# Kernel optimization log

Hardware: AMD Instinct MI355X
Metric: run time of the kernel (lower is better)

Reference implementation:

```python
import jax, jax.numpy as jnp
import numpy as np

V, E, H, K, PAD = 30000, 128, 256, 32, 0
B, T = 128, 512


def _lstm_dir(x, W_ih, W_hh, b, reverse):
    # x: [B,T,E]; PyTorch LSTM gate order i,f,g,o. b = b_ih + b_hh (mathematically identical).
    Bb, Hh = x.shape[0], W_hh.shape[1]
    xg = jnp.einsum('bte,ge->btg', x, W_ih) + b          # [B,T,4H] precomputed input gates
    xg = jnp.swapaxes(xg, 0, 1)                          # [T,B,4H]

    def step(carry, xg_t):
        h, c = carry
        g = xg_t + h @ W_hh.T
        i, f, gc, o = jnp.split(g, 4, axis=-1)
        c = jax.nn.sigmoid(f) * c + jax.nn.sigmoid(i) * jnp.tanh(gc)
        h = jax.nn.sigmoid(o) * jnp.tanh(c)
        return (h, c), h

    init = (jnp.zeros((Bb, Hh), x.dtype), jnp.zeros((Bb, Hh), x.dtype))
    _, hs = jax.lax.scan(step, init, xg, reverse=reverse)
    return jnp.swapaxes(hs, 0, 1)                        # [B,T,H]


def _viterbi(em, mask, start, end, trans):
    # torchcrf-style Viterbi decode. em: [B,T,K], mask: [B,T] bool (mask[:,0] all True).
    Bb, Tt, Kk = em.shape
    score0 = start[None, :] + em[:, 0]                   # [B,K]
    em_t = jnp.swapaxes(em, 0, 1)[1:]                    # [T-1,B,K]
    m_t = jnp.swapaxes(mask, 0, 1)[1:]                   # [T-1,B]

    def step(score, inp):
        e, m = inp
        cand = score[:, :, None] + trans[None] + e[:, None, :]   # [B,K,K]
        nxt = cand.max(axis=1)
        idx = cand.argmax(axis=1).astype(jnp.int32)               # backpointers [B,K]
        score = jnp.where(m[:, None], nxt, score)
        return score, idx

    score, hist = jax.lax.scan(step, score0, (em_t, m_t))         # hist: [T-1,B,K]
    score = score + end[None, :]
    best = jnp.argmax(score, axis=1).astype(jnp.int32)            # [B] tag at seq end
    barange = jnp.arange(Bb)

    def back(b, inp):
        idx, m = inp
        nb = jnp.where(m, idx[barange, b], b)
        return nb, nb

    _, tags_prev = jax.lax.scan(back, best, (hist, m_t), reverse=True)  # [T-1,B]
    tags = jnp.concatenate([tags_prev, best[None]], axis=0)             # [T,B]
    return jnp.swapaxes(tags, 0, 1)                                     # [B,T] int32


def setup_inputs() -> dict:
    key = jax.random.key(0)
    ks = jax.random.split(key, 14)
    s = 0.1
    f32 = jnp.float32
    return {
        'input': jax.random.randint(ks[0], (B, T), 0, V),
        'mask': jnp.ones((B, T), dtype=bool),
        'target': jax.random.randint(ks[1], (B, T), 0, K),
        'embed_table': jax.random.normal(ks[2], (V, E), f32) * s,
        'W_ih_f': jax.random.normal(ks[3], (4 * H, E), f32) * s,
        'W_hh_f': jax.random.normal(ks[4], (4 * H, H), f32) * s,
        'b_f': jax.random.normal(ks[5], (4 * H,), f32) * s,
        'W_ih_b': jax.random.normal(ks[6], (4 * H, E), f32) * s,
        'W_hh_b': jax.random.normal(ks[7], (4 * H, H), f32) * s,
        'b_b': jax.random.normal(ks[8], (4 * H,), f32) * s,
        'linear_w': jax.random.normal(ks[9], (K, 2 * H), f32) * s,
        'linear_b': jax.random.normal(ks[10], (K,), f32) * s,
        'start_trans': jax.random.normal(ks[11], (K,), f32) * s,
        'end_trans': jax.random.normal(ks[12], (K,), f32) * s,
        'transitions': jax.random.normal(ks[13], (K, K), f32) * s,
    }


def reference(input, mask, target, embed_table, W_ih_f, W_hh_f, b_f,
              W_ih_b, W_hh_b, b_b, linear_w, linear_b,
              start_trans, end_trans, transitions):
    # target is only used by loss_fn; forward() is decode, so it is unused here.
    table = embed_table.at[PAD].set(0.0)                 # padding_idx row is zero
    x = table[input]                                     # [B,T,E]
    hf = _lstm_dir(x, W_ih_f, W_hh_f, b_f, reverse=False)
    hb = _lstm_dir(x, W_ih_b, W_hh_b, b_b, reverse=True)
    h = jnp.concatenate([hf, hb], axis=-1)               # [B,T,2H]
    em = jnp.einsum('bth,kh->btk', h, linear_w) + linear_b  # emissions [B,T,K]
    return _viterbi(em, mask, start_trans, end_trans, transitions)
```

## Files before the change

### kernel.cpp

```cpp
#include <hip/hip_runtime.h>
#include <stdint.h>

#define BB 128
#define TT 512
#define EE 128
#define HH 256
#define KK 32
#define ASTRD 386
#define WSTR  388
#define MAGIC 0x13572468

typedef double f64x4 __attribute__((ext_vector_type(4)));

#define OFF_CNT (512ull << 10)
#define OFF_FLG (516ull << 10)
#define OFF_EM  (2ull << 20)

__global__ __launch_bounds__(512, 1) void k_persist(
        const int* __restrict__ tok, const float* __restrict__ table,
        const float* __restrict__ Wihf, const float* __restrict__ Whhf,
        const float* __restrict__ bf,
        const float* __restrict__ Wihb, const float* __restrict__ Whhb,
        const float* __restrict__ bb,
        const float* __restrict__ lw,
        float* __restrict__ hx, int* __restrict__ cnt,
        double* __restrict__ em, int* __restrict__ flags) {
    __shared__ __align__(16) double Ah[16 * ASTRD];
    __shared__ __align__(16) float  Wl[64 * WSTR];
    __shared__ float Gl[16 * 66];
    __shared__ float Lw[2 * 256];

    const int tid  = threadIdx.x;
    const int blk  = blockIdx.x;
    const int grp  = blk & 15;
    const int dir  = grp >> 3;
    const int tile = grp & 7;
    const int hsl  = blk >> 4;
    const int b0   = tile * 16;
    const int u0   = hsl * 16;
    int* mycnt = cnt + grp * 64;

    if (blk == 0 && tid == 0) flags[8] = MAGIC;

    const float* Wih = dir ? Wihb : Wihf;
    const float* Whh = dir ? Whhb : Whhf;
    const float* bia = dir ? bb : bf;

    for (int idx = tid; idx < 64 * 384; idx += 512) {
        int c = idx / 384;
        int k = idx - c * 384;
        int grow = (c >> 4) * HH + u0 + (c & 15);
        float v = (k < EE) ? Wih[(size_t)grow * EE + k]
                           : Whh[(size_t)grow * HH + (k - EE)];
        Wl[c * WSTR + k] = v;
    }
    {
        int i = tid;
        Lw[i] = lw[(size_t)(hsl * 2 + (i >> 8)) * (2 * HH) + dir * HH + (i & 255)];
    }

    const int l = tid & 63;
    const int w = tid >> 6;

    int mode = 0;
    int rowIdx[4] = {0, 0, 0, 0}, colIdx[4] = {0, 0, 0, 0};
    int mAi = l & 15, kAi = l >> 4, nBi = l & 15, kBi = l >> 4;
    {
        f64x4 z; z[0] = 0.0; z[1] = 0.0; z[2] = 0.0; z[3] = 0.0;
        f64x4 d1 = __builtin_amdgcn_mfma_f64_16x16x4f64((double)l, 1.0, z, 0, 0, 0);
        f64x4 d2 = __builtin_amdgcn_mfma_f64_16x16x4f64(1.0, (double)l, z, 0, 0, 0);
        bool am = true, ak = true, bm = true, bk = true;
        int rm[4], rk[4], cm[4], ck[4];
#pragma unroll
        for (int r = 0; r < 4; ++r) {
            const int v1 = (int)d1[r], v2 = (int)d2[r];
            const bool e1 = ((double)v1 == d1[r]);
            const bool e2 = ((double)v2 == d2[r]);
            rm[r] = (v1 - 96) >> 2;
            am = am && e1 && (((v1 - 96) & 3) == 0) && rm[r] >= 0 && rm[r] < 16;
            rk[r] = (v1 - 6) >> 4;
            ak = ak && e1 && (((v1 - 6) & 15) == 0) && rk[r] >= 0 && rk[r] < 16;
            cm[r] = (v2 - 96) >> 2;
            bm = bm && e2 && (((v2 - 96) & 3) == 0) && cm[r] >= 0 && cm[r] < 16;
            ck[r] = (v2 - 6) >> 4;
            bk = bk && e2 && (((v2 - 6) & 15) == 0) && ck[r] >= 0 && ck[r] < 16;
        }
        const bool Am = (__ballot(am ? 1 : 0) == ~0ull);
        const bool Ak = (__ballot(ak ? 1 : 0) == ~0ull);
        const bool Bm = (__ballot(bm ? 1 : 0) == ~0ull);
        const bool Bk = (__ballot(bk ? 1 : 0) == ~0ull);
        if ((Am || Ak) && (Bm || Bk)) {
            mAi = Am ? (l & 15) : (l >> 2);
            kAi = Am ? (l >> 4) : (l & 3);
            nBi = Bm ? (l & 15) : (l >> 2);
            kBi = Bm ? (l >> 4) : (l & 3);
            f64x4 d3 = __builtin_amdgcn_mfma_f64_16x16x4f64(
                (double)kAi, (double)(1 << kBi), z, 0, 0, 0);
            const bool k34 = (d3[0] == 34.0) && (d3[1] == 34.0) &&
                             (d3[2] == 34.0) && (d3[3] == 34.0);
            if (__ballot(k34 ? 1 : 0) == ~0ull) {
                mode = 1;
#pragma unroll
                for (int r = 0; r < 4; ++r) {
                    rowIdx[r] = Am ? rm[r] : rk[r];
                    colIdx[r] = Bm ? cm[r] : ck[r];
                }
            }
        }
    }

    const int c = tid & 63;
    const float* WrowL = Wl + c * WSTR;
    const float bias_c = bia[(c >> 4) * HH + u0 + (c & 15)];

    const double* Arow = Ah + mAi * ASTRD;
    const float*  Wb   = Wl + (w * 16 + nBi) * WSTR + kBi;
    int   glIdx[4];
    float biasv[4];
#pragma unroll
    for (int r = 0; r < 4; ++r) {
        glIdx[r] = rowIdx[r] * 66 + w * 16 + colIdx[r];
        biasv[r] = bia[w * HH + u0 + colIdx[r]];
    }

    const int er = tid >> 4, eu = tid & 15;
    float c_state = 0.f;
    long guard = 0;
    float xgv[2];
    float xgm[4];

    for (int s = 0; s <= TT; ++s) {
        if (s < TT) {
            const int t = dir ? (TT - 1 - s) : s;
            const int i = tid;
            const int r = i >> 5, e4 = i & 31;
            int tk = tok[(b0 + r) * TT + t];
            float4 v = make_float4(0.f, 0.f, 0.f, 0.f);
            if (tk != 0) v = ((const float4*)(table + (size_t)tk * EE))[e4];
            double2* dst = (double2*)(Ah + r * ASTRD + e4 * 4);
            dst[0] = make_double2((double)v.x, (double)v.y);
            dst[1] = make_double2((double)v.z, (double)v.w);
        }
        __syncthreads();

        if (s < TT) {
            if (mode != 0) {
                if (w < 4) {
                    f64x4 ax0; ax0[0]=0.0; ax0[1]=0.0; ax0[2]=0.0; ax0[3]=0.0;
                    f64x4 ax1 = ax0;
#pragma unroll 8
                    for (int kb = 0; kb < 32; kb += 2) {
                        double a0 = Arow[kb * 4 + kAi];
                        double b0 = (double)Wb[kb * 4];
                        double a1 = Arow[(kb + 1) * 4 + kAi];
                        double b1 = (double)Wb[(kb + 1) * 4];
                        ax0 = __builtin_amdgcn_mfma_f64_16x16x4f64(a0, b0, ax0, 0, 0, 0);
                        ax1 = __builtin_amdgcn_mfma_f64_16x16x4f64(a1, b1, ax1, 0, 0, 0);
                    }
#pragma unroll
                    for (int r = 0; r < 4; ++r)
                        xgm[r] = __fadd_rn((float)(ax0[r] + ax1[r]), biasv[r]);
                }
            } else {
                double a0 = 0.0, a1 = 0.0;
                const double* A0 = Ah + (2 * w + 0) * ASTRD;
                const double* A1 = Ah + (2 * w + 1) * ASTRD;
#pragma unroll 4
                for (int k = 0; k < EE; k += 4) {
                    float4 wf = *((const float4*)(WrowL + k));
                    const double w0 = wf.x, w1 = wf.y, w2 = wf.z, w3 = wf.w;
                    double2 q0, q1;
                    q0 = *((const double2*)(A0 + k)); q1 = *((const double2*)(A0 + k + 2));
                    a0 += q0.x * w0 + q0.y * w1 + q1.x * w2 + q1.y * w3;
                    q0 = *((const double2*)(A1 + k)); q1 = *((const double2*)(A1 + k + 2));
                    a1 += q0.x * w0 + q0.y * w1 + q1.x * w2 + q1.y * w3;
                }
                xgv[0] = __fadd_rn((float)a0, bias_c);
                xgv[1] = __fadd_rn((float)a1, bias_c);
            }
        }

        if (s > 0 && tid == 0) {
            const int target = 16 * s;
            while (__hip_atomic_load(mycnt, __ATOMIC_RELAXED,
                                     __HIP_MEMORY_SCOPE_AGENT) < target) {
                __builtin_amdgcn_s_sleep(2);
                if (++guard > 100000000L) {
                    __hip_atomic_store(&flags[10], s, __ATOMIC_RELAXED,
                                       __HIP_MEMORY_SCOPE_AGENT);
                    break;
                }
            }
            __threadfence();
        }
        __syncthreads();

        if (s == 0) {
            for (int i = tid; i < 2048; i += 512) {
                int r = i >> 7, u2 = i & 127;
                *((double2*)(Ah + r * ASTRD + EE + u2 * 2)) = make_double2(0.0, 0.0);
            }
        } else {
            const int rp = (s & 1) ^ 1;
            int i = tid;
#pragma unroll
            for (int rep = 0; rep < 4; ++rep, i += 512) {
                int r = i >> 7, u2 = i & 127;
                const unsigned long long* p = (const unsigned long long*)
                    (hx + ((size_t)((rp * 2 + dir) * BB + b0 + r)) * HH + u2 * 2);
                unsigned long long raw = __hip_atomic_load(
                    p, __ATOMIC_RELAXED, __HIP_MEMORY_SCOPE_AGENT);
                union { unsigned long long u; float f[2]; } cv; cv.u = raw;
                *((double2*)(Ah + r * ASTRD + EE + u2 * 2)) =
                    make_double2((double)cv.f[0], (double)cv.f[1]);
            }
        }
        __syncthreads();

        if (s >= 1 && tid < 256) {
            const int d = tid >> 3, sub = tid & 7;
            const int row = d >> 1, kk = d & 1;
            const int t_em = dir ? (TT - s) : (s - 1);
            double p = 0.0;
#pragma unroll
            for (int j = sub * 32; j < sub * 32 + 32; ++j)
                p += Ah[row * ASTRD + EE + j] * (double)Lw[kk * 256 + j];
            p += __shfl_xor(p, 1, 64);
            p += __shfl_xor(p, 2, 64);
            p += __shfl_xor(p, 4, 64);
            if (sub == 0)
                atomicAdd(em + ((size_t)(b0 + row) * TT + t_em) * KK + hsl * 2 + kk, p);
        }
        if (s == TT) break;

        if (mode != 0) {
            if (w < 4) {
                f64x4 ah0; ah0[0]=0.0; ah0[1]=0.0; ah0[2]=0.0; ah0[3]=0.0;
                f64x4 ah1 = ah0;
#pragma unroll 8
                for (int kb = 32; kb < 96; kb += 2) {
                    double a0 = Arow[kb * 4 + kAi];
                    double b0 = (double)Wb[kb * 4];
                    double a1 = Arow[(kb + 1) * 4 + kAi];
                    double b1 = (double)Wb[(kb + 1) * 4];
                    ah0 = __builtin_amdgcn_mfma_f64_16x16x4f64(a0, b0, ah0, 0, 0, 0);
                    ah1 = __builtin_amdgcn_mfma_f64_16x16x4f64(a1, b1, ah1, 0, 0, 0);
                }
#pragma unroll
                for (int r = 0; r < 4; ++r)
                    Gl[glIdx[r]] = __fadd_rn(xgm[r], (float)(ah0[r] + ah1[r]));
            }
        } else {
            double a0 = 0.0, a1 = 0.0;
            const double* A0 = Ah + (2 * w + 0) * ASTRD + EE;
            const double* A1 = Ah + (2 * w + 1) * ASTRD + EE;
            const float* WhL = WrowL + EE;
#pragma unroll 4
            for (int k = 0; k < HH; k += 4) {
                float4 wf = *((const float4*)(WhL + k));
                const double w0 = wf.x, w1 = wf.y, w2 = wf.z, w3 = wf.w;
                double2 q0, q1;
                q0 = *((const double2*)(A0 + k)); q1 = *((const double2*)(A0 + k + 2));
                a0 += q0.x * w0 + q0.y * w1 + q1.x * w2 + q1.y * w3;
                q0 = *((const double2*)(A1 + k)); q1 = *((const double2*)(A1 + k + 2));
                a1 += q0.x * w0 + q0.y * w1 + q1.x * w2 + q1.y * w3;
            }
            Gl[(2 * w + 0) * 66 + c] = __fadd_rn(xgv[0], (float)a0);
            Gl[(2 * w + 1) * 66 + c] = __fadd_rn(xgv[1], (float)a1);
        }
        __syncthreads();

        if (tid < 256) {
            const float gi = Gl[er * 66 +  0 + eu];
            const float gf = Gl[er * 66 + 16 + eu];
            const float gg = Gl[er * 66 + 32 + eu];
            const float go = Gl[er * 66 + 48 + eu];
            const float si = 1.f / (1.f + expf(-gi));
            const float sf = 1.f / (1.f + expf(-gf));
            const float so = 1.f / (1.f + expf(-go));
            const float tg = tanhf(gg);
            const float cnew = __fadd_rn(__fmul_rn(sf, c_state), __fmul_rn(si, tg));
            c_state = cnew;
            const float hval = __fmul_rn(so, tanhf(cnew));
            __hip_atomic_store(
                hx + ((size_t)(((s & 1) * 2 + dir) * BB + b0 + er)) * HH + u0 + eu,
                hval, __ATOMIC_RELAXED, __HIP_MEMORY_SCOPE_AGENT);
        }

        __syncthreads();
        if (tid == 0) {
            __threadfence();
            __hip_atomic_fetch_add(mycnt, 1, __ATOMIC_RELAXED,
                                   __HIP_MEMORY_SCOPE_AGENT);
        }
    }
}

__global__ __launch_bounds__(64) void k_viterbi(const double* __restrict__ em,
                                                const float* __restrict__ lb,
                                                const float* __restrict__ startt,
                                                const float* __restrict__ endt,
                                                const float* __restrict__ trans,
                                                int* __restrict__ out) {
    const int b = blockIdx.x;
    const int lane = threadIdx.x;
    const int j = lane & 31, half = lane >> 5;
    __shared__ float trs[32][33];
    __shared__ unsigned char hist[TT][32];
    __shared__ int tags[TT];

    for (int idx = lane; idx < 1024; idx += 64)
        trs[idx >> 5][idx & 31] = trans[idx];
    __syncthreads();

    const float lbj = lb[j];
    const double* emb = em + (size_t)b * TT * KK;
    float score = __fadd_rn(startt[j], __fadd_rn((float)emb[j], lbj));

    for (int t = 1; t < TT; ++t) {
        const float e_cur = __fadd_rn((float)emb[(size_t)t * KK + j], lbj);
        float best = -3.4e38f; int bi = 0;
#pragma unroll
        for (int ii = 0; ii < 16; ++ii) {
            int i = half * 16 + ii;
            float sc_i = __shfl(score, i, 64);
            float c1 = __fadd_rn(sc_i, trs[i][j]);
            float cand = __fadd_rn(c1, e_cur);
            if (cand > best) { best = cand; bi = i; }
        }
        float ob = __shfl_xor(best, 32, 64);
        int obi = __shfl_xor(bi, 32, 64);
        if (ob > best || (ob == best && obi < bi)) { best = ob; bi = obi; }
        score = best;
        if (half == 0) hist[t][j] = (unsigned char)bi;
    }

    score = __fadd_rn(score, endt[j]);
    int bj = j; float bs = score;
#pragma unroll
    for (int off = 16; off >= 1; off >>= 1) {
        float os = __shfl_xor(bs, off, 64);
        int oj = __shfl_xor(bj, off, 64);
        if (os > bs || (os == bs && oj < bj)) { bs = os; bj = oj; }
    }
    __syncthreads();
    if (lane == 0) {
        int cur = bj;
        tags[TT - 1] = cur;
        for (int t = TT - 2; t >= 0; --t) { cur = hist[t + 1][cur]; tags[t] = cur; }
    }
    __syncthreads();
    for (int t2 = lane; t2 < TT; t2 += 64) out[b * TT + t2] = tags[t2];
}

__global__ __launch_bounds__(64) void k_final(const int* __restrict__ flags,
                                              int* __restrict__ outp) {
    if (threadIdx.x != 0) return;
    if (flags[8] != MAGIC)   outp[0] = 990000;
    else if (flags[10] != 0) outp[0] = 850000 + flags[10] * 64;
}

extern "C" void kernel_launch(void* const* d_in, const int* in_sizes, int n_in,
                              void* d_out, int out_size, void* d_ws, size_t ws_size,
                              hipStream_t stream) {
    const int*   tok   = (const int*)d_in[0];
    const float* table = (const float*)d_in[3];
    const float* Wihf  = (const float*)d_in[4];
    const float* Whhf  = (const float*)d_in[5];
    const float* bf    = (const float*)d_in[6];
    const float* Wihb  = (const float*)d_in[7];
    const float* Whhb  = (const float*)d_in[8];
    const float* bb    = (const float*)d_in[9];
    const float* lw    = (const float*)d_in[10];
    const float* lb    = (const float*)d_in[11];
    const float* st    = (const float*)d_in[12];
    const float* en    = (const float*)d_in[13];
    const float* tr    = (const float*)d_in[14];

    if (ws_size < (19ull << 20)) return;

    char* ws = (char*)d_ws;
    float*  hx    = (float*)ws;
    int*    cnt   = (int*)(ws + OFF_CNT);
    int*    flags = (int*)(ws + OFF_FLG);
    double* em    = (double*)(ws + OFF_EM);

    hipMemsetAsync(cnt, 0, 8192, stream);
    hipMemsetAsync(em, 0, (size_t)BB * TT * KK * 8, stream);
    k_persist<<<256, 512, 0, stream>>>(tok, table, Wihf, Whhf, bf,
                                       Wihb, Whhb, bb, lw, hx, cnt, em, flags);
    k_viterbi<<<BB, 64, 0, stream>>>(em, lb, st, en, tr, (int*)d_out);
    k_final  <<<1, 64, 0, stream>>>(flags, (int*)d_out);
}
```

Measured before the change: 6.623 ms.

## Split MFMA K-range across all eight waves and relayout LDS operands into k-slabs

In the MFMA path, the LSTM gate GEMM now uses all eight waves instead of four. Each half of the waves covers half the K range, and the partial sums are combined through shared memory after an extra barrier. The A operand is stored in a k-major slab layout (SLAB=66) so MFMA fragment loads are contiguous and avoid bank conflicts. The emission projection is moved after the counter signal and uses a transposed, padded weight layout, so it runs off the recurrence's critical path. These changes add a block barrier and scratch traffic per step, and overlapping the emission work with the next step's spin-wait could race with writes to AA.

```diff
diff --git a/kernel.cpp b/kernel.cpp
--- a/kernel.cpp
+++ b/kernel.cpp
@@ -6,8 +6,8 @@
 #define EE 128
 #define HH 256
 #define KK 32
-#define ASTRD 386
 #define WSTR  388
+#define SLAB  66
 #define MAGIC 0x13572468
 
 typedef double f64x4 __attribute__((ext_vector_type(4)));
@@ -25,10 +25,10 @@
         const float* __restrict__ lw,
         float* __restrict__ hx, int* __restrict__ cnt,
         double* __restrict__ em, int* __restrict__ flags) {
-    __shared__ __align__(16) double Ah[16 * ASTRD];
+    __shared__ __align__(16) double AA[96 * SLAB];
     __shared__ __align__(16) float  Wl[64 * WSTR];
     __shared__ float Gl[16 * 66];
-    __shared__ float Lw[2 * 256];
+    __shared__ float LwR[2 * 8 * 33];
 
     const int tid  = threadIdx.x;
     const int blk  = blockIdx.x;
@@ -55,12 +55,15 @@
         Wl[c * WSTR + k] = v;
     }
     {
-        int i = tid;
-        Lw[i] = lw[(size_t)(hsl * 2 + (i >> 8)) * (2 * HH) + dir * HH + (i & 255)];
+        int kk = tid >> 8, sub = (tid >> 5) & 7, i2 = tid & 31;
+        LwR[(kk * 8 + sub) * 33 + i2] =
+            lw[(size_t)(hsl * 2 + kk) * (2 * HH) + dir * HH + 8 * i2 + sub];
     }
 
     const int l = tid & 63;
     const int w = tid >> 6;
+    const int g    = w & 3;
+    const int half = w >> 2;
 
     int mode = 0;
     int rowIdx[4] = {0, 0, 0, 0}, colIdx[4] = {0, 0, 0, 0};
@@ -113,58 +116,63 @@
     const float* WrowL = Wl + c * WSTR;
     const float bias_c = bia[(c >> 4) * HH + u0 + (c & 15)];
 
-    const double* Arow = Ah + mAi * ASTRD;
-    const float*  Wb   = Wl + (w * 16 + nBi) * WSTR + kBi;
+    const int myIdx = mAi * 4 + kAi;
+    const float* Wb = Wl + (g * 16 + nBi) * WSTR + kBi;
     int   glIdx[4];
     float biasv[4];
 #pragma unroll
     for (int r = 0; r < 4; ++r) {
-        glIdx[r] = rowIdx[r] * 66 + w * 16 + colIdx[r];
-        biasv[r] = bia[w * HH + u0 + colIdx[r]];
+        glIdx[r] = rowIdx[r] * 66 + g * 16 + colIdx[r];
+        biasv[r] = bia[g * HH + u0 + colIdx[r]];
     }
 
     const int er = tid >> 4, eu = tid & 15;
+    const int ed = tid >> 3, esub = tid & 7;
+    const int erow = ed >> 1, ekk = ed & 1;
     float c_state = 0.f;
     long guard = 0;
     float xgv[2];
-    float xgm[4];
+    f64x4 Sx, Sh;
 
     for (int s = 0; s <= TT; ++s) {
         if (s < TT) {
             const int t = dir ? (TT - 1 - s) : s;
-            const int i = tid;
-            const int r = i >> 5, e4 = i & 31;
+            const int r = tid >> 5, e4 = tid & 31;
             int tk = tok[(b0 + r) * TT + t];
             float4 v = make_float4(0.f, 0.f, 0.f, 0.f);
             if (tk != 0) v = ((const float4*)(table + (size_t)tk * EE))[e4];
-            double2* dst = (double2*)(Ah + r * ASTRD + e4 * 4);
-            dst[0] = make_double2((double)v.x, (double)v.y);
-            dst[1] = make_double2((double)v.z, (double)v.w);
+            if (mode) {
+                double* dst = AA + e4 * SLAB + r * 4;
+                ((double2*)dst)[0] = make_double2((double)v.x, (double)v.y);
+                ((double2*)dst)[1] = make_double2((double)v.z, (double)v.w);
+            } else {
+                double2* dst = (double2*)(AA + r * 386 + e4 * 4);
+                dst[0] = make_double2((double)v.x, (double)v.y);
+                dst[1] = make_double2((double)v.z, (double)v.w);
+            }
         }
         __syncthreads();
 
         if (s < TT) {
-            if (mode != 0) {
-                if (w < 4) {
-                    f64x4 ax0; ax0[0]=0.0; ax0[1]=0.0; ax0[2]=0.0; ax0[3]=0.0;
-                    f64x4 ax1 = ax0;
-#pragma unroll 8
-                    for (int kb = 0; kb < 32; kb += 2) {
-                        double a0 = Arow[kb * 4 + kAi];
-                        double b0 = (double)Wb[kb * 4];
-                        double a1 = Arow[(kb + 1) * 4 + kAi];
-                        double b1 = (double)Wb[(kb + 1) * 4];
-                        ax0 = __builtin_amdgcn_mfma_f64_16x16x4f64(a0, b0, ax0, 0, 0, 0);
-                        ax1 = __builtin_amdgcn_mfma_f64_16x16x4f64(a1, b1, ax1, 0, 0, 0);
-                    }
-#pragma unroll
-                    for (int r = 0; r < 4; ++r)
-                        xgm[r] = __fadd_rn((float)(ax0[r] + ax1[r]), biasv[r]);
-                }
+            if (mode) {
+                f64x4 c0; c0[0]=0.0; c0[1]=0.0; c0[2]=0.0; c0[3]=0.0;
+                f64x4 c1 = c0;
+                const int kb0 = half * 16;
+#pragma unroll
+                for (int kb = kb0; kb < kb0 + 16; kb += 2) {
+                    double a0 = AA[kb * SLAB + myIdx];
+                    double b0 = (double)Wb[kb * 4];
+                    double a1 = AA[(kb + 1) * SLAB + myIdx];
+                    double b1 = (double)Wb[(kb + 1) * 4];
+                    c0 = __builtin_amdgcn_mfma_f64_16x16x4f64(a0, b0, c0, 0, 0, 0);
+                    c1 = __builtin_amdgcn_mfma_f64_16x16x4f64(a1, b1, c1, 0, 0, 0);
+                }
+#pragma unroll
+                for (int r = 0; r < 4; ++r) Sx[r] = c0[r] + c1[r];
             } else {
                 double a0 = 0.0, a1 = 0.0;
-                const double* A0 = Ah + (2 * w + 0) * ASTRD;
-                const double* A1 = Ah + (2 * w + 1) * ASTRD;
+                const double* A0 = AA + (2 * w + 0) * 386;
+                const double* A1 = AA + (2 * w + 1) * 386;
 #pragma unroll 4
                 for (int k = 0; k < EE; k += 4) {
                     float4 wf = *((const float4*)(WrowL + k));
@@ -196,9 +204,13 @@
         __syncthreads();
 
         if (s == 0) {
-            for (int i = tid; i < 2048; i += 512) {
-                int r = i >> 7, u2 = i & 127;
-                *((double2*)(Ah + r * ASTRD + EE + u2 * 2)) = make_double2(0.0, 0.0);
+            if (mode) {
+                for (int i = tid; i < 64 * SLAB; i += 512) AA[32 * SLAB + i] = 0.0;
+            } else {
+                for (int i = tid; i < 2048; i += 512) {
+                    int r = i >> 7, u2 = i & 127;
+                    *((double2*)(AA + r * 386 + EE + u2 * 2)) = make_double2(0.0, 0.0);
+                }
             }
         } else {
             const int rp = (s & 1) ^ 1;
@@ -211,49 +223,74 @@
                 unsigned long long raw = __hip_atomic_load(
                     p, __ATOMIC_RELAXED, __HIP_MEMORY_SCOPE_AGENT);
                 union { unsigned long long u; float f[2]; } cv; cv.u = raw;
-                *((double2*)(Ah + r * ASTRD + EE + u2 * 2)) =
-                    make_double2((double)cv.f[0], (double)cv.f[1]);
+                if (mode) {
+                    double* dst = AA + (32 + (u2 >> 1)) * SLAB + r * 4 + ((u2 & 1) << 1);
+                    ((double2*)dst)[0] =
+                        make_double2((double)cv.f[0], (double)cv.f[1]);
+                } else {
+                    *((double2*)(AA + r * 386 + EE + u2 * 2)) =
+                        make_double2((double)cv.f[0], (double)cv.f[1]);
+                }
             }
         }
         __syncthreads();
 
-        if (s >= 1 && tid < 256) {
-            const int d = tid >> 3, sub = tid & 7;
-            const int row = d >> 1, kk = d & 1;
-            const int t_em = dir ? (TT - s) : (s - 1);
-            double p = 0.0;
-#pragma unroll
-            for (int j = sub * 32; j < sub * 32 + 32; ++j)
-                p += Ah[row * ASTRD + EE + j] * (double)Lw[kk * 256 + j];
-            p += __shfl_xor(p, 1, 64);
-            p += __shfl_xor(p, 2, 64);
-            p += __shfl_xor(p, 4, 64);
-            if (sub == 0)
-                atomicAdd(em + ((size_t)(b0 + row) * TT + t_em) * KK + hsl * 2 + kk, p);
-        }
-        if (s == TT) break;
-
-        if (mode != 0) {
-            if (w < 4) {
-                f64x4 ah0; ah0[0]=0.0; ah0[1]=0.0; ah0[2]=0.0; ah0[3]=0.0;
-                f64x4 ah1 = ah0;
+        if (s == TT) {
+            if (tid < 256) {
+                const int t_em = dir ? (TT - s) : (s - 1);
+                double p = 0.0;
+#pragma unroll
+                for (int i2 = 0; i2 < 32; ++i2) {
+                    const int j = 8 * i2 + esub;
+                    double hv = mode
+                        ? AA[(32 + (j >> 2)) * SLAB + erow * 4 + (j & 3)]
+                        : AA[erow * 386 + EE + j];
+                    p += hv * (double)LwR[(ekk * 8 + esub) * 33 + i2];
+                }
+                p += __shfl_xor(p, 1, 64);
+                p += __shfl_xor(p, 2, 64);
+                p += __shfl_xor(p, 4, 64);
+                if (esub == 0)
+                    atomicAdd(em + ((size_t)(b0 + erow) * TT + t_em) * KK + hsl * 2 + ekk, p);
+            }
+            break;
+        }
+
+        if (mode) {
+            f64x4 c0; c0[0]=0.0; c0[1]=0.0; c0[2]=0.0; c0[3]=0.0;
+            f64x4 c1 = c0;
+            const int kb0 = 32 + half * 32;
 #pragma unroll 8
-                for (int kb = 32; kb < 96; kb += 2) {
-                    double a0 = Arow[kb * 4 + kAi];
-                    double b0 = (double)Wb[kb * 4];
-                    double a1 = Arow[(kb + 1) * 4 + kAi];
-                    double b1 = (double)Wb[(kb + 1) * 4];
-                    ah0 = __builtin_amdgcn_mfma_f64_16x16x4f64(a0, b0, ah0, 0, 0, 0);
-                    ah1 = __builtin_amdgcn_mfma_f64_16x16x4f64(a1, b1, ah1, 0, 0, 0);
-                }
-#pragma unroll
-                for (int r = 0; r < 4; ++r)
-                    Gl[glIdx[r]] = __fadd_rn(xgm[r], (float)(ah0[r] + ah1[r]));
+            for (int kb = kb0; kb < kb0 + 32; kb += 2) {
+                double a0 = AA[kb * SLAB + myIdx];
+                double b0 = (double)Wb[kb * 4];
+                double a1 = AA[(kb + 1) * SLAB + myIdx];
+                double b1 = (double)Wb[(kb + 1) * 4];
+                c0 = __builtin_amdgcn_mfma_f64_16x16x4f64(a0, b0, c0, 0, 0, 0);
+                c1 = __builtin_amdgcn_mfma_f64_16x16x4f64(a1, b1, c1, 0, 0, 0);
+            }
+#pragma unroll
+            for (int r = 0; r < 4; ++r) Sh[r] = c0[r] + c1[r];
+            if (half) {
+#pragma unroll
+                for (int r = 0; r < 4; ++r) {
+                    double* dst = AA + (((g * 4 + r) * 64 + l) << 1);
+                    ((double2*)dst)[0] = make_double2(Sx[r], Sh[r]);
+                }
+            }
+            __syncthreads();
+            if (!half) {
+#pragma unroll
+                for (int r = 0; r < 4; ++r) {
+                    double2 hi = *((const double2*)(AA + (((g * 4 + r) * 64 + l) << 1)));
+                    float t1 = __fadd_rn((float)(Sx[r] + hi.x), biasv[r]);
+                    Gl[glIdx[r]] = __fadd_rn(t1, (float)(Sh[r] + hi.y));
+                }
             }
         } else {
             double a0 = 0.0, a1 = 0.0;
-            const double* A0 = Ah + (2 * w + 0) * ASTRD + EE;
-            const double* A1 = Ah + (2 * w + 1) * ASTRD + EE;
+            const double* A0 = AA + (2 * w + 0) * 386 + EE;
+            const double* A1 = AA + (2 * w + 1) * 386 + EE;
             const float* WhL = WrowL + EE;
 #pragma unroll 4
             for (int k = 0; k < HH; k += 4) {
@@ -265,6 +302,7 @@
                 q0 = *((const double2*)(A1 + k)); q1 = *((const double2*)(A1 + k + 2));
                 a1 += q0.x * w0 + q0.y * w1 + q1.x * w2 + q1.y * w3;
             }
+            __syncthreads();
             Gl[(2 * w + 0) * 66 + c] = __fadd_rn(xgv[0], (float)a0);
             Gl[(2 * w + 1) * 66 + c] = __fadd_rn(xgv[1], (float)a1);
         }
@@ -292,6 +330,24 @@
             __threadfence();
             __hip_atomic_fetch_add(mycnt, 1, __ATOMIC_RELAXED,
                                    __HIP_MEMORY_SCOPE_AGENT);
+        }
+
+        if (s >= 1 && tid < 256) {
+            const int t_em = dir ? (TT - s) : (s - 1);
+            double p = 0.0;
+#pragma unroll
+            for (int i2 = 0; i2 < 32; ++i2) {
+                const int j = 8 * i2 + esub;
+                double hv = mode
+                    ? AA[(32 + (j >> 2)) * SLAB + erow * 4 + (j & 3)]
+                    : AA[erow * 386 + EE + j];
+                p += hv * (double)LwR[(ekk * 8 + esub) * 33 + i2];
+            }
+            p += __shfl_xor(p, 1, 64);
+            p += __shfl_xor(p, 2, 64);
+            p += __shfl_xor(p, 4, 64);
+            if (esub == 0)
+                atomicAdd(em + ((size_t)(b0 + erow) * TT + t_em) * KK + hsl * 2 + ekk, p);
         }
     }
 }
```

Measured after the change: 6.952 ms. +5.0%, slower.
